# Kernel tuning notes

Measured on AMD Instinct MI355X. Metric: run time of the kernel, lower is better.

The kernel has to match this reference:

```python
import jax, jax.numpy as jnp
import numpy as np

IN_FEATURES = 4096
OUT_FEATURES = 4096
NNZ = 838860
BATCH = 512


def setup_inputs() -> dict:
    key = jax.random.key(0)
    kx, kr, kc, kv, kb = jax.random.split(key, 5)
    x = jax.random.normal(kx, (BATCH, IN_FEATURES), dtype=jnp.float32)
    row_idx = jax.random.randint(kr, (NNZ,), 0, OUT_FEATURES, dtype=jnp.int64)
    col_idx = jax.random.randint(kc, (NNZ,), 0, IN_FEATURES, dtype=jnp.int64)
    values = jax.random.normal(kv, (NNZ,), dtype=jnp.float32)
    bias = jax.random.normal(kb, (OUT_FEATURES,), dtype=jnp.float32)
    return {"x": x, "row_idx": row_idx, "col_idx": col_idx,
            "values": values, "bias": bias}


def reference(x, row_idx, col_idx, values, bias):
    # COO sparse linear: y[b, row] += x[b, col] * val, then add bias.
    x_flat = x.reshape(-1, IN_FEATURES)                    # [B, in]
    weighted = x_flat[:, col_idx] * values                 # [B, nnz]
    out = jnp.zeros((x_flat.shape[0], OUT_FEATURES), dtype=x.dtype)
    out = out.at[:, row_idx].add(weighted)                 # scatter-add per row
    out = out + bias
    return out.reshape(x.shape[:-1] + (OUT_FEATURES,))
```

## Files before the change

### kernel.cpp

```cpp
#include <hip/hip_runtime.h>

#define IN_F    4096
#define OUT_F   4096
#define K_DIM   4096
#define NNZ_C   838860
#define BATCH   512
#define BK      32
#define BM      128
#define BN      128

typedef short bf16x8 __attribute__((ext_vector_type(8)));
typedef float f32x4  __attribute__((ext_vector_type(4)));

__device__ __forceinline__ unsigned short f2bf(float f) {
    unsigned u = __float_as_uint(f);
    u += 0x7fffu + ((u >> 16) & 1u);
    return (unsigned short)(u >> 16);
}
__device__ __forceinline__ void gload_lds16(const void* g, void* l) {
    __builtin_amdgcn_global_load_lds(
        (const __attribute__((address_space(1))) unsigned int*)g,
        (__attribute__((address_space(3))) unsigned int*)l, 16, 0, 0);
}


#define N_CVT   (BATCH * K_DIM / 8)
#define N_OUT   (BATCH * OUT_F / 4)
#define NS_BLK  ((NNZ_C / 4 + 255) / 256)
#define NC_BLK  (N_CVT / 256)
#define NB_BLK  (N_OUT / 256)
__global__ void scatcvt(const int* __restrict__ row_idx,
                        const int* __restrict__ col_idx,
                        const float* __restrict__ values,
                        unsigned short* __restrict__ W,
                        const float* __restrict__ x,
                        unsigned short* __restrict__ xb,
                        const float* __restrict__ bias,
                        float* __restrict__ out) {
    int b = blockIdx.x;
    if (b < NS_BLK) {
        int i = b * 256 + threadIdx.x;
        if (i >= NNZ_C / 4) return;
        int4   r4 = ((const int4*)row_idx)[i];
        int4   c4 = ((const int4*)col_idx)[i];
        float4 v4 = ((const float4*)values)[i];
#pragma unroll
        for (int j = 0; j < 4; ++j) {
            int r = (&r4.x)[j], c = (&c4.x)[j];
            float v = (&v4.x)[j];
            unsigned idx = (unsigned)r * K_DIM + (unsigned)c;
            unsigned short h = f2bf(v);
            unsigned data = (idx & 1u) ? ((unsigned)h << 16) : (unsigned)h;
            unsigned long long addr = (unsigned long long)(W + (idx & ~1u));
            asm volatile("global_atomic_pk_add_bf16 %0, %1, off"
                         :: "v"(addr), "v"(data) : "memory");
        }
        return;
    }
    b -= NS_BLK;
    if (b < NC_BLK) {
        int i = b * 256 + threadIdx.x;
        const float4* p = (const float4*)x + (size_t)i * 2;
        float4 a = p[0], bb = p[1];
        union { unsigned short h[8]; bf16x8 v; } u;
        u.h[0] = f2bf(a.x);  u.h[1] = f2bf(a.y);  u.h[2] = f2bf(a.z);  u.h[3] = f2bf(a.w);
        u.h[4] = f2bf(bb.x); u.h[5] = f2bf(bb.y); u.h[6] = f2bf(bb.z); u.h[7] = f2bf(bb.w);
        ((bf16x8*)xb)[i] = u.v;
        return;
    }
    b -= NC_BLK;
    int i = b * 256 + threadIdx.x;
    if (i < N_OUT) {
        float4 bb = ((const float4*)bias)[i & (OUT_F / 4 - 1)];
        ((float4*)out)[i] = bb;
    }
}

template <int SK>
__global__ void __launch_bounds__(512)
gemm_at(const unsigned short* __restrict__ Abf,
        const unsigned short* __restrict__ Wbf,
        float* __restrict__ out) {
    __shared__ __align__(16) unsigned short As[2][BM * BK];
    __shared__ __align__(16) unsigned short Bs[2][BN * BK];

    const int nt = blockIdx.x, mt = blockIdx.y, s = blockIdx.z;
    const int t = threadIdx.x, w = t >> 6, ln = t & 63;
    const int wm = w & 1, wn = w >> 1;
    const int KSs = K_DIM / SK;
    const int ks0 = s * KSs;

    const int srow = w * 16 + (ln >> 2);
    const int scol = (((ln & 3) ^ ((ln >> 3) & 3)) * 8);
    const unsigned short* gA0 = Abf + (size_t)(mt * BM + srow) * K_DIM + ks0 + scol;
    const unsigned short* gB0 = Wbf + (size_t)(nt * BN + srow) * K_DIM + ks0 + scol;
    const int lA0o = (w * 16) * BK;

    const int quad = ln >> 4, lanem = ln & 15;
    const int rsw = (quad ^ ((lanem >> 1) & 3)) * 8;
    const int rAo = (wm * 64 + lanem) * BK + rsw;
    const int rBo = (wn * 32 + lanem) * BK + rsw;

    f32x4 acc[4][2];
#pragma unroll
    for (int mi = 0; mi < 4; ++mi)
#pragma unroll
        for (int ni = 0; ni < 2; ++ni)
            acc[mi][ni] = (f32x4){0.f, 0.f, 0.f, 0.f};

    auto stage = [&](int kt) {
#pragma unroll
        for (int ks = 0; ks < 2; ++ks) {
            const int off = kt * 64 + ks * BK;
            gload_lds16(gA0 + off, &As[ks][lA0o]);
            gload_lds16(gB0 + off, &Bs[ks][lA0o]);
        }
    };

    const int NK = KSs / 64;
    stage(0);
    for (int kt = 0; kt < NK; ++kt) {
        __syncthreads();
#pragma unroll
        for (int ks = 0; ks < 2; ++ks) {
            const unsigned short* rA = &As[ks][0] + rAo;
            const unsigned short* rB = &Bs[ks][0] + rBo;
            bf16x8 af[4], bfr[2];
#pragma unroll
            for (int mi = 0; mi < 4; ++mi) af[mi]  = *(const bf16x8*)(rA + mi * 16 * BK);
#pragma unroll
            for (int ni = 0; ni < 2; ++ni) bfr[ni] = *(const bf16x8*)(rB + ni * 16 * BK);
#pragma unroll
            for (int mi = 0; mi < 4; ++mi)
#pragma unroll
                for (int ni = 0; ni < 2; ++ni)
                    acc[mi][ni] = __builtin_amdgcn_mfma_f32_16x16x32_bf16(
                        af[mi], bfr[ni], acc[mi][ni], 0, 0, 0);
        }
        __syncthreads();
        if (kt + 1 < NK) stage(kt + 1);
    }

    const int row0 = mt * BM + wm * 64 + quad * 4;
    const int col0 = nt * BN + wn * 32 + lanem;
#pragma unroll
    for (int mi = 0; mi < 4; ++mi)
#pragma unroll
        for (int ni = 0; ni < 2; ++ni)
#pragma unroll
            for (int r = 0; r < 4; ++r)
                atomicAdd(&out[(size_t)(row0 + mi * 16 + r) * OUT_F + col0 + ni * 16],
                          acc[mi][ni][r]);
}

extern "C" void kernel_launch(void* const* d_in, const int* in_sizes, int n_in,
                              void* d_out, int out_size, void* d_ws, size_t ws_size,
                              hipStream_t stream) {
    const float* x       = (const float*)d_in[0];
    const int*   row_idx = (const int*)d_in[1];
    const int*   col_idx = (const int*)d_in[2];
    const float* values  = (const float*)d_in[3];
    const float* bias    = (const float*)d_in[4];
    float*       out     = (float*)d_out;

    unsigned short* xb = (unsigned short*)d_ws;
    unsigned short* W  = xb + (size_t)BATCH * K_DIM;

    hipMemsetAsync(W, 0, (size_t)OUT_F * K_DIM * 2, stream);

    scatcvt<<<NS_BLK + NC_BLK + NB_BLK, 256, 0, stream>>>(
        row_idx, col_idx, values, W, x, xb, bias, out);

    gemm_at<4><<<dim3(OUT_F / BN, BATCH / BM, 4), 512, 0, stream>>>(xb, W, out);
}
```

Baseline: 162.2 us.

## Replace grid split-K atomics with intra-block K-split and LDS reduction

The GEMM switches from 128x128 tiles with a 4-way split-K across the grid and global atomicAdd to 64x64 tiles where the two halves of each 512-thread block cover separate K halves. The halves are combined through LDS, and bias is added in the epilogue with plain stores. This drops the bias pre-fill of the output and the global float atomics, and hipMemsetAsync is replaced with a custom zeroing kernel. The cost is smaller tiles, so each A and W element is reloaded from global memory more often, while the grid of 512 blocks keeps the same parallelism.

```diff
diff --git a/kernel.cpp b/kernel.cpp
--- a/kernel.cpp
+++ b/kernel.cpp
@@ -6,8 +6,9 @@
 #define NNZ_C   838860
 #define BATCH   512
 #define BK      32
-#define BM      128
-#define BN      128
+#define TM      64
+#define TN      64
+#define KH      (K_DIM / 2)
 
 typedef short bf16x8 __attribute__((ext_vector_type(8)));
 typedef float f32x4  __attribute__((ext_vector_type(4)));
@@ -24,19 +25,22 @@
 }
 
 
+#define N_WZ   (OUT_F * K_DIM / 8)
+__global__ void zero_w(uint4* __restrict__ Wz) {
+    int i = blockIdx.x * 256 + threadIdx.x;
+    Wz[i] = make_uint4(0, 0, 0, 0);
+}
+#define ZW_BLOCKS (N_WZ / 256)
+
 #define N_CVT   (BATCH * K_DIM / 8)
-#define N_OUT   (BATCH * OUT_F / 4)
 #define NS_BLK  ((NNZ_C / 4 + 255) / 256)
 #define NC_BLK  (N_CVT / 256)
-#define NB_BLK  (N_OUT / 256)
 __global__ void scatcvt(const int* __restrict__ row_idx,
                         const int* __restrict__ col_idx,
                         const float* __restrict__ values,
                         unsigned short* __restrict__ W,
                         const float* __restrict__ x,
-                        unsigned short* __restrict__ xb,
-                        const float* __restrict__ bias,
-                        float* __restrict__ out) {
+                        unsigned short* __restrict__ xb) {
     int b = blockIdx.x;
     if (b < NS_BLK) {
         int i = b * 256 + threadIdx.x;
@@ -58,7 +62,7 @@
         return;
     }
     b -= NS_BLK;
-    if (b < NC_BLK) {
+    {
         int i = b * 256 + threadIdx.x;
         const float4* p = (const float4*)x + (size_t)i * 2;
         float4 a = p[0], bb = p[1];
@@ -66,44 +70,38 @@
         u.h[0] = f2bf(a.x);  u.h[1] = f2bf(a.y);  u.h[2] = f2bf(a.z);  u.h[3] = f2bf(a.w);
         u.h[4] = f2bf(bb.x); u.h[5] = f2bf(bb.y); u.h[6] = f2bf(bb.z); u.h[7] = f2bf(bb.w);
         ((bf16x8*)xb)[i] = u.v;
-        return;
-    }
-    b -= NC_BLK;
-    int i = b * 256 + threadIdx.x;
-    if (i < N_OUT) {
-        float4 bb = ((const float4*)bias)[i & (OUT_F / 4 - 1)];
-        ((float4*)out)[i] = bb;
     }
 }
 
-template <int SK>
 __global__ void __launch_bounds__(512)
-gemm_at(const unsigned short* __restrict__ Abf,
-        const unsigned short* __restrict__ Wbf,
-        float* __restrict__ out) {
-    __shared__ __align__(16) unsigned short As[2][BM * BK];
-    __shared__ __align__(16) unsigned short Bs[2][BN * BK];
+gemm_ksplit(const unsigned short* __restrict__ Abf,
+            const unsigned short* __restrict__ Wbf,
+            const float* __restrict__ bias,
+            float* __restrict__ out) {
+    __shared__ __align__(16) unsigned short As[2][2][TM * BK];
+    __shared__ __align__(16) unsigned short Bs[2][2][TN * BK];
 
-    const int nt = blockIdx.x, mt = blockIdx.y, s = blockIdx.z;
+    const int nt = blockIdx.x, mt = blockIdx.y;
     const int t = threadIdx.x, w = t >> 6, ln = t & 63;
-    const int wm = w & 1, wn = w >> 1;
-    const int KSs = K_DIM / SK;
-    const int ks0 = s * KSs;
+    const int wm = w & 1, wn = (w >> 1) & 1;
+    const int kg = w >> 2;
+    const int wsub = w & 3;
+    const int ks0 = kg * KH;
 
-    const int srow = w * 16 + (ln >> 2);
+    const int srow = wsub * 16 + (ln >> 2);
     const int scol = (((ln & 3) ^ ((ln >> 3) & 3)) * 8);
-    const unsigned short* gA0 = Abf + (size_t)(mt * BM + srow) * K_DIM + ks0 + scol;
-    const unsigned short* gB0 = Wbf + (size_t)(nt * BN + srow) * K_DIM + ks0 + scol;
-    const int lA0o = (w * 16) * BK;
+    const unsigned short* gA0 = Abf + (size_t)(mt * TM + srow) * K_DIM + ks0 + scol;
+    const unsigned short* gB0 = Wbf + (size_t)(nt * TN + srow) * K_DIM + ks0 + scol;
+    const int lro = (wsub * 16) * BK;
 
     const int quad = ln >> 4, lanem = ln & 15;
     const int rsw = (quad ^ ((lanem >> 1) & 3)) * 8;
-    const int rAo = (wm * 64 + lanem) * BK + rsw;
+    const int rAo = (wm * 32 + lanem) * BK + rsw;
     const int rBo = (wn * 32 + lanem) * BK + rsw;
 
-    f32x4 acc[4][2];
+    f32x4 acc[2][2];
 #pragma unroll
-    for (int mi = 0; mi < 4; ++mi)
+    for (int mi = 0; mi < 2; ++mi)
 #pragma unroll
         for (int ni = 0; ni < 2; ++ni)
             acc[mi][ni] = (f32x4){0.f, 0.f, 0.f, 0.f};
@@ -112,26 +110,26 @@
 #pragma unroll
         for (int ks = 0; ks < 2; ++ks) {
             const int off = kt * 64 + ks * BK;
-            gload_lds16(gA0 + off, &As[ks][lA0o]);
-            gload_lds16(gB0 + off, &Bs[ks][lA0o]);
+            gload_lds16(gA0 + off, &As[kg][ks][lro]);
+            gload_lds16(gB0 + off, &Bs[kg][ks][lro]);
         }
     };
 
-    const int NK = KSs / 64;
+    const int NK = KH / 64;
     stage(0);
     for (int kt = 0; kt < NK; ++kt) {
         __syncthreads();
 #pragma unroll
         for (int ks = 0; ks < 2; ++ks) {
-            const unsigned short* rA = &As[ks][0] + rAo;
-            const unsigned short* rB = &Bs[ks][0] + rBo;
-            bf16x8 af[4], bfr[2];
+            const unsigned short* rA = &As[kg][ks][0] + rAo;
+            const unsigned short* rB = &Bs[kg][ks][0] + rBo;
+            bf16x8 af[2], bfr[2];
 #pragma unroll
-            for (int mi = 0; mi < 4; ++mi) af[mi]  = *(const bf16x8*)(rA + mi * 16 * BK);
+            for (int mi = 0; mi < 2; ++mi) af[mi]  = *(const bf16x8*)(rA + mi * 16 * BK);
 #pragma unroll
             for (int ni = 0; ni < 2; ++ni) bfr[ni] = *(const bf16x8*)(rB + ni * 16 * BK);
 #pragma unroll
-            for (int mi = 0; mi < 4; ++mi)
+            for (int mi = 0; mi < 2; ++mi)
 #pragma unroll
                 for (int ni = 0; ni < 2; ++ni)
                     acc[mi][ni] = __builtin_amdgcn_mfma_f32_16x16x32_bf16(
@@ -141,16 +139,35 @@
         if (kt + 1 < NK) stage(kt + 1);
     }
 
-    const int row0 = mt * BM + wm * 64 + quad * 4;
-    const int col0 = nt * BN + wn * 32 + lanem;
+    float* xch = (float*)&As[0][0][0];
+    const int lrow = wm * 32 + quad * 4;
+    const int lcol = wn * 32 + lanem;
+    if (kg == 0) {
 #pragma unroll
-    for (int mi = 0; mi < 4; ++mi)
+        for (int mi = 0; mi < 2; ++mi)
 #pragma unroll
-        for (int ni = 0; ni < 2; ++ni)
+            for (int ni = 0; ni < 2; ++ni)
 #pragma unroll
-            for (int r = 0; r < 4; ++r)
-                atomicAdd(&out[(size_t)(row0 + mi * 16 + r) * OUT_F + col0 + ni * 16],
-                          acc[mi][ni][r]);
+                for (int r = 0; r < 4; ++r)
+                    xch[(lrow + mi * 16 + r) * TN + lcol + ni * 16] = acc[mi][ni][r];
+    }
+    __syncthreads();
+    if (kg == 1) {
+        const int row0 = mt * TM + lrow;
+        const int col0 = nt * TN + lcol;
+        float bv[2];
+#pragma unroll
+        for (int ni = 0; ni < 2; ++ni) bv[ni] = bias[col0 + ni * 16];
+#pragma unroll
+        for (int mi = 0; mi < 2; ++mi)
+#pragma unroll
+            for (int ni = 0; ni < 2; ++ni)
+#pragma unroll
+                for (int r = 0; r < 4; ++r)
+                    out[(size_t)(row0 + mi * 16 + r) * OUT_F + col0 + ni * 16] =
+                        acc[mi][ni][r] + bv[ni]
+                        + xch[(lrow + mi * 16 + r) * TN + lcol + ni * 16];
+    }
 }
 
 extern "C" void kernel_launch(void* const* d_in, const int* in_sizes, int n_in,
@@ -166,10 +183,11 @@
     unsigned short* xb = (unsigned short*)d_ws;
     unsigned short* W  = xb + (size_t)BATCH * K_DIM;
 
-    hipMemsetAsync(W, 0, (size_t)OUT_F * K_DIM * 2, stream);
+    zero_w<<<ZW_BLOCKS, 256, 0, stream>>>((uint4*)W);
 
-    scatcvt<<<NS_BLK + NC_BLK + NB_BLK, 256, 0, stream>>>(
-        row_idx, col_idx, values, W, x, xb, bias, out);
+    scatcvt<<<NS_BLK + NC_BLK, 256, 0, stream>>>(row_idx, col_idx, values, W,
+                                                 x, xb);
 
-    gemm_at<4><<<dim3(OUT_F / BN, BATCH / BM, 4), 512, 0, stream>>>(xb, W, out);
+    gemm_ksplit<<<dim3(OUT_F / TN, BATCH / TM), 512, 0, stream>>>(
+        xb, W, bias, out);
 }
```

Measured after the change: 149.4 us. 7.9% less time.
